# Kernel optimization log

Measured on AMD Instinct MI355X. Metric: run time of the kernel, lower is better.

The kernel has to match this reference:

```python
import jax, jax.numpy as jnp
import numpy as np

N = 50000      # nodes
E = 400000     # edges (before self-loops)
DIN = 128
HID = 128
HEADS = 4
DOUT = 64
NEG_SLOPE = 0.2  # PyG GATConv default


def setup_inputs() -> dict:
    key = jax.random.key(0)
    ks = jax.random.split(key, 14)

    def w(k, shape, fan_in):
        return jax.random.normal(k, shape, dtype=jnp.float32) * (1.0 / np.sqrt(fan_in))

    x = jax.random.normal(ks[0], (N, DIN), dtype=jnp.float32)
    edge_index = jax.random.randint(ks[1], (2, E), 0, N, dtype=jnp.int32)

    # layer 1: DIN -> HEADS*HID (concat)
    W1 = w(ks[2], (DIN, HEADS * HID), DIN)
    a_src1 = w(ks[3], (HEADS, HID), HID)
    a_dst1 = w(ks[4], (HEADS, HID), HID)
    b1 = jnp.zeros((HEADS * HID,), jnp.float32)
    # layer 2: HEADS*HID -> HEADS*HID (concat)
    W2 = w(ks[5], (HEADS * HID, HEADS * HID), HEADS * HID)
    a_src2 = w(ks[6], (HEADS, HID), HID)
    a_dst2 = w(ks[7], (HEADS, HID), HID)
    b2 = jnp.zeros((HEADS * HID,), jnp.float32)
    # layer 3: HEADS*HID -> DOUT, heads=1, concat=False (mean)
    W3 = w(ks[8], (HEADS * HID, DOUT), HEADS * HID)
    a_src3 = w(ks[9], (1, DOUT), DOUT)
    a_dst3 = w(ks[10], (1, DOUT), DOUT)
    b3 = jnp.zeros((DOUT,), jnp.float32)

    return dict(x=x, edge_index=edge_index,
                W1=W1, a_src1=a_src1, a_dst1=a_dst1, b1=b1,
                W2=W2, a_src2=a_src2, a_dst2=a_dst2, b2=b2,
                W3=W3, a_src3=a_src3, a_dst3=a_dst3, b3=b3)


def _gat_layer(x, src, dst, W, a_src, a_dst, n):
    """One GATConv (eval mode, self-loops already in src/dst). Returns [n, H, C]."""
    H, C = a_src.shape
    h = (x @ W).reshape(n, H, C)                        # projected features
    alpha_s = jnp.einsum('nhc,hc->nh', h, a_src)        # per-node src logits
    alpha_d = jnp.einsum('nhc,hc->nh', h, a_dst)
    e = jax.nn.leaky_relu(alpha_s[src] + alpha_d[dst], NEG_SLOPE)  # [E', H]
    # segment softmax over incoming edges of each dst node
    m = jax.ops.segment_max(e, dst, num_segments=n)
    e = jnp.exp(e - m[dst])
    s = jax.ops.segment_sum(e, dst, num_segments=n)
    alpha = e / (s[dst] + 1e-16)                        # [E', H]
    msg = h[src] * alpha[:, :, None]                    # [E', H, C]
    return jax.ops.segment_sum(msg, dst, num_segments=n)


def reference(x, edge_index, W1, a_src1, a_dst1, b1,
              W2, a_src2, a_dst2, b2, W3, a_src3, a_dst3, b3):
    n = x.shape[0]
    loops = jnp.arange(n, dtype=edge_index.dtype)       # PyG add_self_loops=True
    src = jnp.concatenate([edge_index[0], loops])
    dst = jnp.concatenate([edge_index[1], loops])

    h = _gat_layer(x, src, dst, W1, a_src1, a_dst1, n).reshape(n, -1) + b1
    h = jax.nn.elu(h)   # dropout is identity in eval mode
    h = _gat_layer(h, src, dst, W2, a_src2, a_dst2, n).reshape(n, -1) + b2
    h = jax.nn.elu(h)
    out = _gat_layer(h, src, dst, W3, a_src3, a_dst3, n)[:, 0, :] + b3  # heads=1, concat=False
    return out
```

## Files before the change

### kernel.cpp

```cpp
#include <hip/hip_runtime.h>
#include <hip/hip_bf16.h>


typedef __attribute__((ext_vector_type(8))) short bf16x8;
typedef __attribute__((ext_vector_type(4))) float f32x4;

__device__ __forceinline__ float bflo(unsigned w) { return __uint_as_float(w << 16); }
__device__ __forceinline__ float bfhi(unsigned w) { return __uint_as_float(w & 0xffff0000u); }
__device__ __forceinline__ float leaky(float x) { return x > 0.f ? x : 0.2f * x; }
__device__ __forceinline__ unsigned pack2(float a, float b) {
    unsigned ua = __bfloat16_as_ushort(__float2bfloat16(a));
    unsigned ub = __bfloat16_as_ushort(__float2bfloat16(b));
    return ua | (ub << 16);
}


__global__ void k_count(const int* __restrict__ ei, int E, int N, int* __restrict__ cnt) {
    int e = blockIdx.x * blockDim.x + threadIdx.x;
    int tot = E + N;
    if (e >= tot) return;
    int d = (e < E) ? ei[E + e] : (e - E);
    atomicAdd(&cnt[d], 1);
}

__global__ void k_scan1(const int* __restrict__ cnt, int N, int* __restrict__ rp,
                        int* __restrict__ blksum) {
    __shared__ int sdata[256];
    int t = threadIdx.x;
    int base = blockIdx.x * 1024;
    int v[4];
    int loc = 0;
#pragma unroll
    for (int i = 0; i < 4; i++) {
        int idx = base + t * 4 + i;
        v[i] = (idx < N) ? ((cnt[idx] + 3) & ~3) : 0;
        loc += v[i];
    }
    int x = loc;
    sdata[t] = x;
    __syncthreads();
    for (int off = 1; off < 256; off <<= 1) {
        int y = (t >= off) ? sdata[t - off] : 0;
        __syncthreads();
        x += y;
        sdata[t] = x;
        __syncthreads();
    }
    int run = x - loc;
#pragma unroll
    for (int i = 0; i < 4; i++) {
        int idx = base + t * 4 + i;
        if (idx < N) rp[idx] = run;
        run += v[i];
    }
    if (t == 255) blksum[blockIdx.x] = x;
}

__global__ void k_scan2(const int* __restrict__ blksum, int nblk, int* __restrict__ blkoff) {
    int l = threadIdx.x;
    int v = (l < nblk) ? blksum[l] : 0;
    int x = v;
#pragma unroll
    for (int off = 1; off < 64; off <<= 1) {
        int y = __shfl_up(x, off);
        if (l >= off) x += y;
    }
    if (l < nblk) blkoff[l] = x - v;
}

__global__ void k_scan3(int* __restrict__ rp, const int* __restrict__ blkoff,
                        const int* __restrict__ blksum, const int* __restrict__ cnt,
                        int N, int nblk, int* __restrict__ cur,
                        int* __restrict__ col, int* __restrict__ dste) {
    int i = blockIdx.x * blockDim.x + threadIdx.x;
    if (i < N) {
        int v = rp[i] + blkoff[i >> 10];
        rp[i] = v;
        cur[i] = v;
        int c = cnt[i];
        int pad = ((c + 3) & ~3) - c;
        for (int p = 0; p < pad; p++) {
            col[v + c + p] = 0;
            dste[v + c + p] = -1;
        }
    }
    if (i == 0) rp[N] = blkoff[nblk - 1] + blksum[nblk - 1];
}

__global__ void k_fill(const int* __restrict__ ei, int E, int N, int* __restrict__ cur,
                       int* __restrict__ col, int* __restrict__ dste) {
    int e = blockIdx.x * blockDim.x + threadIdx.x;
    int tot = E + N;
    if (e >= tot) return;
    int s, d;
    if (e < E) { s = ei[e]; d = ei[E + e]; }
    else       { s = e - E; d = e - E; }
    int p = atomicAdd(&cur[d], 1);
    col[p] = s;
    dste[p] = d;
}


__global__ void k_cast_alpha(const float* __restrict__ X, __hip_bfloat16* __restrict__ Xb,
                             const float* __restrict__ va8, float* __restrict__ as_out,
                             float* __restrict__ ad_out, int N, int Mp) {
    int w = (blockIdx.x * blockDim.x + threadIdx.x) >> 6;
    int lane = threadIdx.x & 63;
    if (w >= Mp) return;
    unsigned* xb32 = (unsigned*)Xb;
    if (w >= N) {
        xb32[(size_t)w * 64 + lane] = 0u;
        return;
    }
    float2 xv = *(const float2*)&X[(size_t)w * 128 + lane * 2];
    xb32[(size_t)w * 64 + lane] = pack2(xv.x, xv.y);
    int c0 = lane * 2;
    float4 vs0 = *(const float4*)&va8[c0 * 8];
    float4 vd0 = *(const float4*)&va8[c0 * 8 + 4];
    float4 vs1 = *(const float4*)&va8[(c0 + 1) * 8];
    float4 vd1 = *(const float4*)&va8[(c0 + 1) * 8 + 4];
    float s[8];
    s[0] = xv.x * vs0.x + xv.y * vs1.x;
    s[1] = xv.x * vs0.y + xv.y * vs1.y;
    s[2] = xv.x * vs0.z + xv.y * vs1.z;
    s[3] = xv.x * vs0.w + xv.y * vs1.w;
    s[4] = xv.x * vd0.x + xv.y * vd1.x;
    s[5] = xv.x * vd0.y + xv.y * vd1.y;
    s[6] = xv.x * vd0.z + xv.y * vd1.z;
    s[7] = xv.x * vd0.w + xv.y * vd1.w;
#pragma unroll
    for (int off = 32; off >= 1; off >>= 1)
#pragma unroll
        for (int j = 0; j < 8; j++) s[j] += __shfl_xor(s[j], off);
    if (lane == 0) {
        *(float4*)&as_out[w * 4] = make_float4(s[0], s[1], s[2], s[3]);
        *(float4*)&ad_out[w * 4] = make_float4(s[4], s[5], s[6], s[7]);
    }
}

__global__ void k_castT(const float* __restrict__ W, __hip_bfloat16* __restrict__ Wt,
                        int K, int Nw) {
    __shared__ float t[32][33];
    int k0 = blockIdx.x * 32, n0 = blockIdx.y * 32;
    int tx = threadIdx.x & 31, ty = threadIdx.x >> 5;
    for (int i = ty; i < 32; i += 8) t[i][tx] = W[(size_t)(k0 + i) * Nw + n0 + tx];
    __syncthreads();
    for (int i = ty; i < 32; i += 8)
        Wt[(size_t)(n0 + i) * K + k0 + tx] = __float2bfloat16(t[tx][i]);
}

__global__ void k_va1(const float* __restrict__ W1, const float* __restrict__ asrc,
                      const float* __restrict__ adst, float* __restrict__ va8) {
    int t = threadIdx.x;
    int c = t >> 2, h = t & 3;
    const float* wrow = W1 + (size_t)c * 512 + h * 128;
    const float* av = asrc + h * 128;
    const float* dv = adst + h * 128;
    float vs = 0.f, vd = 0.f;
    for (int k = 0; k < 128; k++) {
        float wv = wrow[k];
        vs += wv * av[k];
        vd += wv * dv[k];
    }
    va8[c * 8 + h] = vs;
    va8[c * 8 + 4 + h] = vd;
}


template <int BM, int BN, bool FUSE, int ALPHA_H>
__global__ void __launch_bounds__(256) k_gemm_mfma(const __hip_bfloat16* __restrict__ A,
                                                   const __hip_bfloat16* __restrict__ Bt,
                                                   __hip_bfloat16* __restrict__ C,
                                                   int lda, int ldc, int K,
                                                   int hsA, int hsB, int hsC,
                                                   const float* __restrict__ bias,
                                                   const float* __restrict__ aSrcTab,
                                                   const float* __restrict__ aDstTab,
                                                   float* __restrict__ asOut,
                                                   float* __restrict__ adOut) {
    constexpr int BK = 64;
    constexpr int WM = BM / 2;
    constexpr int WN = BN / 2;
    constexpr int MREP = WM / 16;
    constexpr int NREP = WN / 16;

    __shared__ __hip_bfloat16 lds[(BM + BN) * BK];
    __hip_bfloat16* As = lds;
    __hip_bfloat16* Bs = lds + BM * BK;

    const int z = blockIdx.z;
    A += (size_t)z * hsA;
    Bt += (size_t)z * hsB;
    const int cbase = z * hsC;

    const int tid = threadIdx.x;
    const int wave = tid >> 6;
    const int lane = tid & 63;
    const int wm0 = (wave >> 1) * WM;
    const int wn0 = (wave & 1) * WN;
    const int m0 = blockIdx.y * BM;
    const int n0 = blockIdx.x * BN;
    const int fr = lane & 15;
    const int fq = lane >> 4;

    f32x4 acc[MREP][NREP] = {};

    for (int kt = 0; kt < K; kt += BK) {
        const __hip_bfloat16* srcA = A + (size_t)m0 * lda + kt;
#pragma unroll
        for (int it = 0; it < BM * 8 / 256; ++it) {
            int gb = it * 256 + wave * 64;
            int g = gb + lane;
            int row = g >> 3;
            int kg = (g & 7) ^ (row & 7);
            const __hip_bfloat16* gsrc = srcA + (size_t)row * lda + kg * 8;
            __builtin_amdgcn_global_load_lds(
                (const __attribute__((address_space(1))) void*)gsrc,
                (__attribute__((address_space(3))) void*)(As + gb * 8), 16, 0, 0);
        }
        const __hip_bfloat16* srcB = Bt + (size_t)n0 * K + kt;
#pragma unroll
        for (int it = 0; it < BN * 8 / 256; ++it) {
            int gb = it * 256 + wave * 64;
            int g = gb + lane;
            int row = g >> 3;
            int kg = (g & 7) ^ (row & 7);
            const __hip_bfloat16* gsrc = srcB + (size_t)row * K + kg * 8;
            __builtin_amdgcn_global_load_lds(
                (const __attribute__((address_space(1))) void*)gsrc,
                (__attribute__((address_space(3))) void*)(Bs + gb * 8), 16, 0, 0);
        }
        __syncthreads();

#pragma unroll
        for (int sl = 0; sl < 2; ++sl) {
            int ke = sl * 32 + fq * 8;
            bf16x8 af[MREP], bfr[NREP];
#pragma unroll
            for (int i = 0; i < MREP; ++i) {
                int row = wm0 + i * 16 + fr;
                int e = (row * BK + ke) ^ ((row & 7) << 3);
                af[i] = *(const bf16x8*)(As + e);
            }
#pragma unroll
            for (int j = 0; j < NREP; ++j) {
                int row = wn0 + j * 16 + fr;
                int e = (row * BK + ke) ^ ((row & 7) << 3);
                bfr[j] = *(const bf16x8*)(Bs + e);
            }
#pragma unroll
            for (int i = 0; i < MREP; ++i)
#pragma unroll
                for (int j = 0; j < NREP; ++j)
                    acc[i][j] = __builtin_amdgcn_mfma_f32_16x16x32_bf16(
                        af[i], bfr[j], acc[i][j], 0, 0, 0);
        }
        __syncthreads();
    }

#pragma unroll
    for (int i = 0; i < MREP; ++i) {
#pragma unroll
        for (int j = 0; j < NREP; ++j) {
            int colg = cbase + n0 + wn0 + j * 16 + fr;
#pragma unroll
            for (int r = 0; r < 4; ++r) {
                int rowg = m0 + wm0 + i * 16 + fq * 4 + r;
                float v = acc[i][j][r];
                if (FUSE) {
                    v += bias[colg];
                    v = v > 0.f ? v : expm1f(v);
                }
                C[(size_t)rowg * ldc + colg] = __float2bfloat16(v);
            }
        }
    }

    if constexpr (ALPHA_H > 0) {
        const int head = (ALPHA_H == 4) ? blockIdx.x : 0;
        float avs[NREP], avd[NREP];
#pragma unroll
        for (int j = 0; j < NREP; ++j) {
            int cl = wn0 + j * 16 + fr;
            avs[j] = aSrcTab[head * BN + cl];
            avd[j] = aDstTab[head * BN + cl];
        }
        float pa[MREP][4] = {};
        float pd_[MREP][4] = {};
#pragma unroll
        for (int i = 0; i < MREP; ++i)
#pragma unroll
            for (int j = 0; j < NREP; ++j)
#pragma unroll
                for (int r = 0; r < 4; ++r) {
                    pa[i][r] += acc[i][j][r] * avs[j];
                    pd_[i][r] += acc[i][j][r] * avd[j];
                }
#pragma unroll
        for (int off = 1; off <= 8; off <<= 1)
#pragma unroll
            for (int i = 0; i < MREP; ++i)
#pragma unroll
                for (int r = 0; r < 4; ++r) {
                    pa[i][r] += __shfl_xor(pa[i][r], off);
                    pd_[i][r] += __shfl_xor(pd_[i][r], off);
                }
        float* lds_a = (float*)lds;
        float* lds_d = lds_a + BM;
        if ((wave & 1) == 0 && fr == 0) {
#pragma unroll
            for (int i = 0; i < MREP; ++i)
#pragma unroll
                for (int r = 0; r < 4; ++r) {
                    int rl = wm0 + i * 16 + fq * 4 + r;
                    lds_a[rl] = pa[i][r];
                    lds_d[rl] = pd_[i][r];
                }
        }
        __syncthreads();
        if ((wave & 1) == 1 && fr == 0) {
#pragma unroll
            for (int i = 0; i < MREP; ++i)
#pragma unroll
                for (int r = 0; r < 4; ++r) {
                    int rl = wm0 + i * 16 + fq * 4 + r;
                    int rowg = m0 + rl;
                    if (ALPHA_H == 4) {
                        asOut[rowg * 4 + head] = lds_a[rl] + pa[i][r];
                        adOut[rowg * 4 + head] = lds_d[rl] + pd_[i][r];
                    } else {
                        asOut[rowg] = lds_a[rl] + pa[i][r];
                        adOut[rowg] = lds_d[rl] + pd_[i][r];
                    }
                }
        }
    }
}


__global__ void k_edgewA(const int* __restrict__ col, const int* __restrict__ dste,
                         const float* __restrict__ as, const float* __restrict__ ad,
                         float* __restrict__ wA, const int* __restrict__ rp, int N) {
    int e = blockIdx.x * blockDim.x + threadIdx.x;
    if (e >= rp[N]) return;
    int d = dste[e];
    if (d < 0) {
        *(float4*)&wA[e * 4] = make_float4(0.f, 0.f, 0.f, 0.f);
        return;
    }
    int s = col[e];
    float4 a = *(const float4*)&as[s * 4];
    float4 b = *(const float4*)&ad[d * 4];
    float4 w;
    w.x = __expf(leaky(a.x + b.x));
    w.y = __expf(leaky(a.y + b.y));
    w.z = __expf(leaky(a.z + b.z));
    w.w = __expf(leaky(a.w + b.w));
    *(float4*)&wA[e * 4] = w;
}


__global__ void k_gatherX(const __hip_bfloat16* __restrict__ xb,
                          const float* __restrict__ wA, const int* __restrict__ rp,
                          const int* __restrict__ col, unsigned* __restrict__ out32, int N) {
    int w = (blockIdx.x * blockDim.x + threadIdx.x) >> 6;
    int lane = threadIdx.x & 63;
    if (w >= N) return;
    int d = w;
    int r0 = rp[d], r1 = rp[d + 1];
    const unsigned* xp = (const unsigned*)xb;

    float acc[8] = {};
    float ws0 = 0.f, ws1 = 0.f, ws2 = 0.f, ws3 = 0.f;
    for (int e = r0; e < r1; e += 4) {
        int4 c4 = *(const int4*)&col[e];
        float4 w0 = *(const float4*)&wA[e * 4];
        float4 w1 = *(const float4*)&wA[e * 4 + 4];
        float4 w2 = *(const float4*)&wA[e * 4 + 8];
        float4 w3 = *(const float4*)&wA[e * 4 + 12];
        unsigned v0 = xp[(size_t)c4.x * 64 + lane];
        unsigned v1 = xp[(size_t)c4.y * 64 + lane];
        unsigned v2 = xp[(size_t)c4.z * 64 + lane];
        unsigned v3 = xp[(size_t)c4.w * 64 + lane];
        ws0 += w0.x + w1.x + w2.x + w3.x;
        ws1 += w0.y + w1.y + w2.y + w3.y;
        ws2 += w0.z + w1.z + w2.z + w3.z;
        ws3 += w0.w + w1.w + w2.w + w3.w;
        float f0, f1;
        f0 = bflo(v0); f1 = bfhi(v0);
        acc[0] += w0.x * f0; acc[1] += w0.x * f1;
        acc[2] += w0.y * f0; acc[3] += w0.y * f1;
        acc[4] += w0.z * f0; acc[5] += w0.z * f1;
        acc[6] += w0.w * f0; acc[7] += w0.w * f1;
        f0 = bflo(v1); f1 = bfhi(v1);
        acc[0] += w1.x * f0; acc[1] += w1.x * f1;
        acc[2] += w1.y * f0; acc[3] += w1.y * f1;
        acc[4] += w1.z * f0; acc[5] += w1.z * f1;
        acc[6] += w1.w * f0; acc[7] += w1.w * f1;
        f0 = bflo(v2); f1 = bfhi(v2);
        acc[0] += w2.x * f0; acc[1] += w2.x * f1;
        acc[2] += w2.y * f0; acc[3] += w2.y * f1;
        acc[4] += w2.z * f0; acc[5] += w2.z * f1;
        acc[6] += w2.w * f0; acc[7] += w2.w * f1;
        f0 = bflo(v3); f1 = bfhi(v3);
        acc[0] += w3.x * f0; acc[1] += w3.x * f1;
        acc[2] += w3.y * f0; acc[3] += w3.y * f1;
        acc[4] += w3.z * f0; acc[5] += w3.z * f1;
        acc[6] += w3.w * f0; acc[7] += w3.w * f1;
    }
    float i0 = 1.f / (ws0 + 1e-16f), i1 = 1.f / (ws1 + 1e-16f);
    float i2 = 1.f / (ws2 + 1e-16f), i3 = 1.f / (ws3 + 1e-16f);
    size_t ob = (size_t)d * 256 + lane;
    out32[ob]       = pack2(acc[0] * i0, acc[1] * i0);
    out32[ob + 64]  = pack2(acc[2] * i1, acc[3] * i1);
    out32[ob + 128] = pack2(acc[4] * i2, acc[5] * i2);
    out32[ob + 192] = pack2(acc[6] * i3, acc[7] * i3);
}


template <bool DO_ELU>
__global__ void k_gather512(const __hip_bfloat16* __restrict__ hfeat,
                            const float* __restrict__ as4, const float* __restrict__ ad4,
                            const int* __restrict__ cnt, const int* __restrict__ rp,
                            const int* __restrict__ col, const float* __restrict__ bias,
                            __hip_bfloat16* __restrict__ out, int N) {
    int w = (blockIdx.x * blockDim.x + threadIdx.x) >> 6;
    int lane = threadIdx.x & 63;
    if (w >= N) return;
    int d = w;
    int r0 = rp[d], r1 = rp[d + 1];
    int r1r = r0 + cnt[d];
    int hd = lane >> 4;
    float adv = ad4[d * 4 + hd];
    const uint4* hp = (const uint4*)hfeat;

    float acc[8] = {};
    float wsum = 0.f;
    for (int e = r0; e < r1; e += 4) {
        int4 c4 = *(const int4*)&col[e];
        float l0 = as4[c4.x * 4 + hd] + adv;
        float l1 = as4[c4.y * 4 + hd] + adv;
        float l2 = as4[c4.z * 4 + hd] + adv;
        float l3 = as4[c4.w * 4 + hd] + adv;
        uint4 v0 = hp[(size_t)c4.x * 64 + lane];
        uint4 v1 = hp[(size_t)c4.y * 64 + lane];
        uint4 v2 = hp[(size_t)c4.z * 64 + lane];
        uint4 v3 = hp[(size_t)c4.w * 64 + lane];
        float w0 = (e + 0 < r1r) ? __expf(leaky(l0)) : 0.f;
        float w1 = (e + 1 < r1r) ? __expf(leaky(l1)) : 0.f;
        float w2 = (e + 2 < r1r) ? __expf(leaky(l2)) : 0.f;
        float w3 = (e + 3 < r1r) ? __expf(leaky(l3)) : 0.f;
        wsum += (w0 + w1) + (w2 + w3);
        acc[0] += w0 * bflo(v0.x); acc[1] += w0 * bfhi(v0.x);
        acc[2] += w0 * bflo(v0.y); acc[3] += w0 * bfhi(v0.y);
        acc[4] += w0 * bflo(v0.z); acc[5] += w0 * bfhi(v0.z);
        acc[6] += w0 * bflo(v0.w); acc[7] += w0 * bfhi(v0.w);
        acc[0] += w1 * bflo(v1.x); acc[1] += w1 * bfhi(v1.x);
        acc[2] += w1 * bflo(v1.y); acc[3] += w1 * bfhi(v1.y);
        acc[4] += w1 * bflo(v1.z); acc[5] += w1 * bfhi(v1.z);
        acc[6] += w1 * bflo(v1.w); acc[7] += w1 * bfhi(v1.w);
        acc[0] += w2 * bflo(v2.x); acc[1] += w2 * bfhi(v2.x);
        acc[2] += w2 * bflo(v2.y); acc[3] += w2 * bfhi(v2.y);
        acc[4] += w2 * bflo(v2.z); acc[5] += w2 * bfhi(v2.z);
        acc[6] += w2 * bflo(v2.w); acc[7] += w2 * bfhi(v2.w);
        acc[0] += w3 * bflo(v3.x); acc[1] += w3 * bfhi(v3.x);
        acc[2] += w3 * bflo(v3.y); acc[3] += w3 * bfhi(v3.y);
        acc[4] += w3 * bflo(v3.z); acc[5] += w3 * bfhi(v3.z);
        acc[6] += w3 * bflo(v3.w); acc[7] += w3 * bfhi(v3.w);
    }

    float inv = 1.0f / (wsum + 1e-16f);
    __hip_bfloat16 tmp[8];
#pragma unroll
    for (int j = 0; j < 8; j++) {
        float v = acc[j] * inv + bias[lane * 8 + j];
        if (DO_ELU) v = v > 0.f ? v : expm1f(v);
        tmp[j] = __float2bfloat16(v);
    }
    *(float4*)(out + (size_t)d * 512 + lane * 8) = *(const float4*)tmp;
}


__global__ void k_gather64(const __hip_bfloat16* __restrict__ hfeat,
                           const float* __restrict__ as1, const float* __restrict__ ad1,
                           const int* __restrict__ cnt, const int* __restrict__ rp,
                           const int* __restrict__ col, const float* __restrict__ bias,
                           float* __restrict__ out, int N) {
    int w = (blockIdx.x * blockDim.x + threadIdx.x) >> 6;
    int lane = threadIdx.x & 63;
    if (w >= N) return;
    int d = w;
    int r0 = rp[d], r1 = rp[d + 1];
    int r1r = r0 + cnt[d];
    float adv = ad1[d];
    int g = lane >> 4, cl = lane & 15;

    float a0 = 0.f, a1 = 0.f, a2 = 0.f, a3 = 0.f, wsum = 0.f;
    for (int e0 = r0; e0 < r1; e0 += 4) {
        int e = e0 + g;
        int s = col[e];
        float l = as1[s] + adv;
        uint2 q = *(const uint2*)(hfeat + (size_t)s * 64 + cl * 4);
        float wf = (e < r1r) ? __expf(leaky(l)) : 0.f;
        wsum += wf;
        a0 += wf * bflo(q.x);
        a1 += wf * bfhi(q.x);
        a2 += wf * bflo(q.y);
        a3 += wf * bfhi(q.y);
    }
#pragma unroll
    for (int off = 16; off <= 32; off <<= 1) {
        a0 += __shfl_xor(a0, off);
        a1 += __shfl_xor(a1, off);
        a2 += __shfl_xor(a2, off);
        a3 += __shfl_xor(a3, off);
        wsum += __shfl_xor(wsum, off);
    }
    if (g == 0) {
        float inv = 1.0f / (wsum + 1e-16f);
        float4 b4 = *(const float4*)&bias[cl * 4];
        float4 o = make_float4(a0 * inv + b4.x, a1 * inv + b4.y,
                               a2 * inv + b4.z, a3 * inv + b4.w);
        *(float4*)(out + (size_t)d * 64 + cl * 4) = o;
    }
}


extern "C" void kernel_launch(void* const* d_in, const int* in_sizes, int n_in,
                              void* d_out, int out_size, void* d_ws, size_t ws_size,
                              hipStream_t stream) {
    const float* x   = (const float*)d_in[0];
    const int*   ei  = (const int*)d_in[1];
    const float* W1  = (const float*)d_in[2];
    const float* as1 = (const float*)d_in[3];
    const float* ad1 = (const float*)d_in[4];
    const float* b1  = (const float*)d_in[5];
    const float* W2  = (const float*)d_in[6];
    const float* as2 = (const float*)d_in[7];
    const float* ad2 = (const float*)d_in[8];
    const float* b2  = (const float*)d_in[9];
    const float* W3  = (const float*)d_in[10];
    const float* as3 = (const float*)d_in[11];
    const float* ad3 = (const float*)d_in[12];
    const float* b3  = (const float*)d_in[13];

    const int N = in_sizes[0] / 128;
    const int E = in_sizes[1] / 2;
    const int Etot = E + N;
    const int EP = (Etot + 3 * N + 255) & ~255;
    const int Mp = (N + 127) & ~127;

    char* ws = (char*)d_ws;
    size_t off = 0;
    auto alloc = [&](size_t bytes) -> void* {
        void* p = ws + off;
        off = (off + bytes + 255) & ~(size_t)255;
        return p;
    };
    __hip_bfloat16* hbuf = (__hip_bfloat16*)alloc((size_t)Mp * 512 * 2);
    __hip_bfloat16* fbuf = (__hip_bfloat16*)alloc((size_t)Mp * 512 * 2);
    __hip_bfloat16* xagg = (__hip_bfloat16*)alloc((size_t)Mp * 512 * 2);
    __hip_bfloat16* xb   = (__hip_bfloat16*)alloc((size_t)Mp * 128 * 2);
    __hip_bfloat16* Wt1  = (__hip_bfloat16*)alloc((size_t)512 * 128 * 2);
    __hip_bfloat16* Wt2  = (__hip_bfloat16*)alloc((size_t)512 * 512 * 2);
    __hip_bfloat16* Wt3  = (__hip_bfloat16*)alloc((size_t)64 * 512 * 2);
    float* aS   = (float*)alloc((size_t)Mp * 4 * 4);
    float* aD   = (float*)alloc((size_t)Mp * 4 * 4);
    float* aS3  = (float*)alloc((size_t)Mp * 4);
    float* aD3  = (float*)alloc((size_t)Mp * 4);
    float* wbuf = (float*)alloc((size_t)EP * 4 * 4);
    float* va8  = (float*)alloc(128 * 8 * 4);
    int* cnt  = (int*)alloc((size_t)N * 4);
    int* rp   = (int*)alloc((size_t)(N + 1) * 4);
    int* cur  = (int*)alloc((size_t)N * 4);
    int* col  = (int*)alloc((size_t)EP * 4);
    int* dste = (int*)alloc((size_t)EP * 4);
    int* blks = (int*)alloc(64 * 4);
    int* blko = (int*)alloc(64 * 4);

    hipMemsetAsync(cnt, 0, (size_t)N * 4, stream);
    int thr = 256;
    k_count<<<(Etot + thr - 1) / thr, thr, 0, stream>>>(ei, E, N, cnt);
    int nblk = (N + 1023) / 1024;
    k_scan1<<<nblk, 256, 0, stream>>>(cnt, N, rp, blks);
    k_scan2<<<1, 64, 0, stream>>>(blks, nblk, blko);
    k_scan3<<<(N + 255) / 256, 256, 0, stream>>>(rp, blko, blks, cnt, N, nblk, cur, col, dste);
    k_fill<<<(Etot + thr - 1) / thr, thr, 0, stream>>>(ei, E, N, cur, col, dste);

    {
        dim3 g1(128 / 32, 512 / 32);
        k_castT<<<g1, 256, 0, stream>>>(W1, Wt1, 128, 512);
        dim3 g2(512 / 32, 512 / 32);
        k_castT<<<g2, 256, 0, stream>>>(W2, Wt2, 512, 512);
        dim3 g3(512 / 32, 64 / 32);
        k_castT<<<g3, 256, 0, stream>>>(W3, Wt3, 512, 64);
        k_va1<<<1, 512, 0, stream>>>(W1, as1, ad1, va8);
        k_cast_alpha<<<(Mp + 3) / 4, 256, 0, stream>>>(x, xb, va8, aS, aD, N, Mp);
    }

    int edgeBlocks = (EP + 255) / 256;
    int gatBlocks = (N + 3) / 4;

    k_edgewA<<<edgeBlocks, 256, 0, stream>>>(col, dste, aS, aD, wbuf, rp, N);
    k_gatherX<<<gatBlocks, 256, 0, stream>>>(xb, wbuf, rp, col, (unsigned*)xagg, N);
    {
        dim3 g(1, Mp / 128, 4);
        k_gemm_mfma<128, 128, true, 0><<<g, 256, 0, stream>>>(
            xagg, Wt1, fbuf, 512, 512, 128, 128, 128 * 128, 128, b1,
            nullptr, nullptr, nullptr, nullptr);
    }

    {
        dim3 g(4, Mp / 128, 1);
        k_gemm_mfma<128, 128, false, 4><<<g, 256, 0, stream>>>(
            fbuf, Wt2, hbuf, 512, 512, 512, 0, 0, 0, nullptr,
            as2, ad2, aS, aD);
    }
    k_gather512<true><<<gatBlocks, 256, 0, stream>>>(hbuf, aS, aD, cnt, rp, col, b2,
                                                     fbuf, N);

    {
        dim3 g(1, Mp / 64, 1);
        k_gemm_mfma<64, 64, false, 1><<<g, 256, 0, stream>>>(
            fbuf, Wt3, hbuf, 512, 64, 512, 0, 0, 0, nullptr,
            as3, ad3, aS3, aD3);
    }
    k_gather64<<<gatBlocks, 256, 0, stream>>>(hbuf, aS3, aD3, cnt, rp, col, b3,
                                              (float*)d_out, N);
}
```

Measured before the change: 384.2 us.

## Fuse layer-1 edge weight computation into gather and merge scan kernels

Removes the separate per-edge attention weight kernel and its float4-per-edge buffer. The layer-1 gather now computes exp(leaky(as+ad)) on the fly, with 16 lanes each handling one edge/head pair and the values broadcast via shuffles, masking padded edges using the true count. This also removes the destination-per-edge array and folds the single-block block-offset scan into the final scan kernel. In exchange, the gather does extra shuffles and exp work, and every scan3 block redundantly computes the 64-entry scan.

New measurement: 377.6 us. No clear change (-1.7%).

```diff
diff --git a/kernel.cpp b/kernel.cpp
--- a/kernel.cpp
+++ b/kernel.cpp
@@ -56,39 +56,36 @@
     if (t == 255) blksum[blockIdx.x] = x;
 }
 
-__global__ void k_scan2(const int* __restrict__ blksum, int nblk, int* __restrict__ blkoff) {
-    int l = threadIdx.x;
-    int v = (l < nblk) ? blksum[l] : 0;
-    int x = v;
-#pragma unroll
-    for (int off = 1; off < 64; off <<= 1) {
-        int y = __shfl_up(x, off);
-        if (l >= off) x += y;
-    }
-    if (l < nblk) blkoff[l] = x - v;
-}
-
-__global__ void k_scan3(int* __restrict__ rp, const int* __restrict__ blkoff,
-                        const int* __restrict__ blksum, const int* __restrict__ cnt,
-                        int N, int nblk, int* __restrict__ cur,
-                        int* __restrict__ col, int* __restrict__ dste) {
+__global__ void k_scan3(int* __restrict__ rp, const int* __restrict__ blksum,
+                        const int* __restrict__ cnt, int N, int nblk,
+                        int* __restrict__ cur, int* __restrict__ col) {
+    __shared__ int lblk[64];
+    if (threadIdx.x < 64) {
+        int l = threadIdx.x;
+        int v = (l < nblk) ? blksum[l] : 0;
+        int x = v;
+#pragma unroll
+        for (int off = 1; off < 64; off <<= 1) {
+            int y = __shfl_up(x, off);
+            if (l >= off) x += y;
+        }
+        lblk[l] = x - v;
+    }
+    __syncthreads();
     int i = blockIdx.x * blockDim.x + threadIdx.x;
     if (i < N) {
-        int v = rp[i] + blkoff[i >> 10];
+        int v = rp[i] + lblk[i >> 10];
         rp[i] = v;
         cur[i] = v;
         int c = cnt[i];
         int pad = ((c + 3) & ~3) - c;
-        for (int p = 0; p < pad; p++) {
-            col[v + c + p] = 0;
-            dste[v + c + p] = -1;
-        }
-    }
-    if (i == 0) rp[N] = blkoff[nblk - 1] + blksum[nblk - 1];
+        for (int p = 0; p < pad; p++) col[v + c + p] = 0;
+    }
+    if (i == 0) rp[N] = lblk[nblk - 1] + blksum[nblk - 1];
 }
 
 __global__ void k_fill(const int* __restrict__ ei, int E, int N, int* __restrict__ cur,
-                       int* __restrict__ col, int* __restrict__ dste) {
+                       int* __restrict__ col) {
     int e = blockIdx.x * blockDim.x + threadIdx.x;
     int tot = E + N;
     if (e >= tot) return;
@@ -97,7 +94,6 @@
     else       { s = e - E; d = e - E; }
     int p = atomicAdd(&cur[d], 1);
     col[p] = s;
-    dste[p] = d;
 }
 
 
@@ -338,75 +334,60 @@
 }
 
 
-__global__ void k_edgewA(const int* __restrict__ col, const int* __restrict__ dste,
-                         const float* __restrict__ as, const float* __restrict__ ad,
-                         float* __restrict__ wA, const int* __restrict__ rp, int N) {
-    int e = blockIdx.x * blockDim.x + threadIdx.x;
-    if (e >= rp[N]) return;
-    int d = dste[e];
-    if (d < 0) {
-        *(float4*)&wA[e * 4] = make_float4(0.f, 0.f, 0.f, 0.f);
-        return;
-    }
-    int s = col[e];
-    float4 a = *(const float4*)&as[s * 4];
-    float4 b = *(const float4*)&ad[d * 4];
-    float4 w;
-    w.x = __expf(leaky(a.x + b.x));
-    w.y = __expf(leaky(a.y + b.y));
-    w.z = __expf(leaky(a.z + b.z));
-    w.w = __expf(leaky(a.w + b.w));
-    *(float4*)&wA[e * 4] = w;
-}
-
-
 __global__ void k_gatherX(const __hip_bfloat16* __restrict__ xb,
-                          const float* __restrict__ wA, const int* __restrict__ rp,
+                          const float* __restrict__ as4, const float* __restrict__ ad4,
+                          const int* __restrict__ cnt, const int* __restrict__ rp,
                           const int* __restrict__ col, unsigned* __restrict__ out32, int N) {
     int w = (blockIdx.x * blockDim.x + threadIdx.x) >> 6;
     int lane = threadIdx.x & 63;
     if (w >= N) return;
     int d = w;
     int r0 = rp[d], r1 = rp[d + 1];
+    int r1r = r0 + cnt[d];
     const unsigned* xp = (const unsigned*)xb;
+    int q = (lane >> 2) & 3, hh = lane & 3;
+    float adv = ad4[d * 4 + hh];
 
     float acc[8] = {};
     float ws0 = 0.f, ws1 = 0.f, ws2 = 0.f, ws3 = 0.f;
     for (int e = r0; e < r1; e += 4) {
         int4 c4 = *(const int4*)&col[e];
-        float4 w0 = *(const float4*)&wA[e * 4];
-        float4 w1 = *(const float4*)&wA[e * 4 + 4];
-        float4 w2 = *(const float4*)&wA[e * 4 + 8];
-        float4 w3 = *(const float4*)&wA[e * 4 + 12];
+        int sq = (q == 0) ? c4.x : (q == 1) ? c4.y : (q == 2) ? c4.z : c4.w;
+        float av = as4[sq * 4 + hh];
+        float wv = (e + q < r1r) ? __expf(leaky(av + adv)) : 0.f;
+        float w00 = __shfl(wv, 0),  w01 = __shfl(wv, 1),  w02 = __shfl(wv, 2),  w03 = __shfl(wv, 3);
+        float w10 = __shfl(wv, 4),  w11 = __shfl(wv, 5),  w12 = __shfl(wv, 6),  w13 = __shfl(wv, 7);
+        float w20 = __shfl(wv, 8),  w21 = __shfl(wv, 9),  w22 = __shfl(wv, 10), w23 = __shfl(wv, 11);
+        float w30 = __shfl(wv, 12), w31 = __shfl(wv, 13), w32 = __shfl(wv, 14), w33 = __shfl(wv, 15);
         unsigned v0 = xp[(size_t)c4.x * 64 + lane];
         unsigned v1 = xp[(size_t)c4.y * 64 + lane];
         unsigned v2 = xp[(size_t)c4.z * 64 + lane];
         unsigned v3 = xp[(size_t)c4.w * 64 + lane];
-        ws0 += w0.x + w1.x + w2.x + w3.x;
-        ws1 += w0.y + w1.y + w2.y + w3.y;
-        ws2 += w0.z + w1.z + w2.z + w3.z;
-        ws3 += w0.w + w1.w + w2.w + w3.w;
+        ws0 += (w00 + w10) + (w20 + w30);
+        ws1 += (w01 + w11) + (w21 + w31);
+        ws2 += (w02 + w12) + (w22 + w32);
+        ws3 += (w03 + w13) + (w23 + w33);
         float f0, f1;
         f0 = bflo(v0); f1 = bfhi(v0);
-        acc[0] += w0.x * f0; acc[1] += w0.x * f1;
-        acc[2] += w0.y * f0; acc[3] += w0.y * f1;
-        acc[4] += w0.z * f0; acc[5] += w0.z * f1;
-        acc[6] += w0.w * f0; acc[7] += w0.w * f1;
+        acc[0] += w00 * f0; acc[1] += w00 * f1;
+        acc[2] += w01 * f0; acc[3] += w01 * f1;
+        acc[4] += w02 * f0; acc[5] += w02 * f1;
+        acc[6] += w03 * f0; acc[7] += w03 * f1;
         f0 = bflo(v1); f1 = bfhi(v1);
-        acc[0] += w1.x * f0; acc[1] += w1.x * f1;
-        acc[2] += w1.y * f0; acc[3] += w1.y * f1;
-        acc[4] += w1.z * f0; acc[5] += w1.z * f1;
-        acc[6] += w1.w * f0; acc[7] += w1.w * f1;
+        acc[0] += w10 * f0; acc[1] += w10 * f1;
+        acc[2] += w11 * f0; acc[3] += w11 * f1;
+        acc[4] += w12 * f0; acc[5] += w12 * f1;
+        acc[6] += w13 * f0; acc[7] += w13 * f1;
         f0 = bflo(v2); f1 = bfhi(v2);
-        acc[0] += w2.x * f0; acc[1] += w2.x * f1;
-        acc[2] += w2.y * f0; acc[3] += w2.y * f1;
-        acc[4] += w2.z * f0; acc[5] += w2.z * f1;
-        acc[6] += w2.w * f0; acc[7] += w2.w * f1;
+        acc[0] += w20 * f0; acc[1] += w20 * f1;
+        acc[2] += w21 * f0; acc[3] += w21 * f1;
+        acc[4] += w22 * f0; acc[5] += w22 * f1;
+        acc[6] += w23 * f0; acc[7] += w23 * f1;
         f0 = bflo(v3); f1 = bfhi(v3);
-        acc[0] += w3.x * f0; acc[1] += w3.x * f1;
-        acc[2] += w3.y * f0; acc[3] += w3.y * f1;
-        acc[4] += w3.z * f0; acc[5] += w3.z * f1;
-        acc[6] += w3.w * f0; acc[7] += w3.w * f1;
+        acc[0] += w30 * f0; acc[1] += w30 * f1;
+        acc[2] += w31 * f0; acc[3] += w31 * f1;
+        acc[4] += w32 * f0; acc[5] += w32 * f1;
+        acc[6] += w33 * f0; acc[7] += w33 * f1;
     }
     float i0 = 1.f / (ws0 + 1e-16f), i1 = 1.f / (ws1 + 1e-16f);
     float i2 = 1.f / (ws2 + 1e-16f), i3 = 1.f / (ws3 + 1e-16f);
@@ -568,24 +549,20 @@
     float* aD   = (float*)alloc((size_t)Mp * 4 * 4);
     float* aS3  = (float*)alloc((size_t)Mp * 4);
     float* aD3  = (float*)alloc((size_t)Mp * 4);
-    float* wbuf = (float*)alloc((size_t)EP * 4 * 4);
     float* va8  = (float*)alloc(128 * 8 * 4);
     int* cnt  = (int*)alloc((size_t)N * 4);
     int* rp   = (int*)alloc((size_t)(N + 1) * 4);
     int* cur  = (int*)alloc((size_t)N * 4);
     int* col  = (int*)alloc((size_t)EP * 4);
-    int* dste = (int*)alloc((size_t)EP * 4);
     int* blks = (int*)alloc(64 * 4);
-    int* blko = (int*)alloc(64 * 4);
 
     hipMemsetAsync(cnt, 0, (size_t)N * 4, stream);
     int thr = 256;
     k_count<<<(Etot + thr - 1) / thr, thr, 0, stream>>>(ei, E, N, cnt);
     int nblk = (N + 1023) / 1024;
     k_scan1<<<nblk, 256, 0, stream>>>(cnt, N, rp, blks);
-    k_scan2<<<1, 64, 0, stream>>>(blks, nblk, blko);
-    k_scan3<<<(N + 255) / 256, 256, 0, stream>>>(rp, blko, blks, cnt, N, nblk, cur, col, dste);
-    k_fill<<<(Etot + thr - 1) / thr, thr, 0, stream>>>(ei, E, N, cur, col, dste);
+    k_scan3<<<(N + 255) / 256, 256, 0, stream>>>(rp, blks, cnt, N, nblk, cur, col);
+    k_fill<<<(Etot + thr - 1) / thr, thr, 0, stream>>>(ei, E, N, cur, col);
 
     {
         dim3 g1(128 / 32, 512 / 32);
@@ -598,11 +575,10 @@
         k_cast_alpha<<<(Mp + 3) / 4, 256, 0, stream>>>(x, xb, va8, aS, aD, N, Mp);
     }
 
-    int edgeBlocks = (EP + 255) / 256;
     int gatBlocks = (N + 3) / 4;
 
-    k_edgewA<<<edgeBlocks, 256, 0, stream>>>(col, dste, aS, aD, wbuf, rp, N);
-    k_gatherX<<<gatBlocks, 256, 0, stream>>>(xb, wbuf, rp, col, (unsigned*)xagg, N);
+    k_gatherX<<<gatBlocks, 256, 0, stream>>>(xb, aS, aD, cnt, rp, col,
+                                             (unsigned*)xagg, N);
     {
         dim3 g(1, Mp / 128, 4);
         k_gemm_mfma<128, 128, true, 0><<<g, 256, 0, stream>>>(
```
